# Optimization experiments

Measured on AMD Instinct MI355X. Metric: run time of the kernel, lower is better.

Reference implementation:

```python
import jax, jax.numpy as jnp
import numpy as np

NUM_HEAD = 16
D = 1024
HEAD_DIM = D // NUM_HEAD
EPS = 1e-5


def setup_inputs() -> dict:
    key = jax.random.key(0)
    ks = jax.random.split(key, 7)
    B, S = 2, 2048
    s = 1.0 / np.sqrt(D)
    return {
        "x": jax.random.normal(ks[0], (B, S, D), dtype=jnp.float32),
        "wq": jax.random.uniform(ks[1], (D, D), jnp.float32, -s, s),
        "bq": jax.random.uniform(ks[2], (D,), jnp.float32, -s, s),
        "wk": jax.random.uniform(ks[3], (D, D), jnp.float32, -s, s),
        "bk": jax.random.uniform(ks[4], (D,), jnp.float32, -s, s),
        "wv": jax.random.uniform(ks[5], (D, D), jnp.float32, -s, s),
        "bv": jax.random.uniform(ks[6], (D,), jnp.float32, -s, s),
        "gamma": jnp.ones((D,), jnp.float32),
        "beta": jnp.zeros((D,), jnp.float32),
    }


def reference(x, wq, bq, wk, bk, wv, bv, gamma, beta):
    B, S, Dm = x.shape
    # Linear: x @ W^T + b (torch convention), then split heads -> [B, H, S, hd]
    def proj(w, b):
        y = jnp.einsum("bsd,ed->bse", x, w) + b
        return y.reshape(B, S, NUM_HEAD, HEAD_DIM).transpose(0, 2, 1, 3)

    q = proj(wq, bq)
    k = proj(wk, bk)
    v = proj(wv, bv)

    scores = jnp.einsum("bhqd,bhkd->bhqk", q, k) / np.sqrt(HEAD_DIM).astype(x.dtype)
    attn = jax.nn.softmax(scores, axis=-1)
    out = jnp.einsum("bhqk,bhkd->bhqd", attn, v)
    out = out.transpose(0, 2, 1, 3).reshape(B, S, Dm)

    out = out + x
    mu = jnp.mean(out, axis=-1, keepdims=True)
    var = jnp.var(out, axis=-1, keepdims=True)
    out = (out - mu) * jax.lax.rsqrt(var + EPS) * gamma + beta
    return out
```

## Files before the change

### kernel.cpp

```cpp
#include <hip/hip_runtime.h>

typedef unsigned short u16;
typedef unsigned int   u32;
typedef __bf16 bf16x8 __attribute__((ext_vector_type(8)));
typedef float  f32x4  __attribute__((ext_vector_type(4)));

#define D_MODEL 1024
#define SEQ     2048
#define NHEAD   16
#define HD      64
#define SOFTMAX_SCL 0.18033688011112042f

__device__ __forceinline__ u16 f2bf(float f) {
    u32 u;
    __builtin_memcpy(&u, &f, 4);
    u32 r = (u + 0x7fffu + ((u >> 16) & 1u)) >> 16;
    return (u16)r;
}
__device__ __forceinline__ float bf2f(u16 v) {
    u32 u = ((u32)v) << 16;
    float f;
    __builtin_memcpy(&f, &u, 4);
    return f;
}

__device__ __forceinline__ void async_copy16(const u16* g, u16* l) {
    __builtin_amdgcn_global_load_lds(
        (__attribute__((address_space(1))) void*)g,
        (__attribute__((address_space(3))) void*)l, 16, 0, 0);
}

#define NX4 ((2 * SEQ * D_MODEL) / 4)
#define NW4 ((D_MODEL * D_MODEL) / 4)
__global__ __launch_bounds__(256) void conv_all(
    const float* __restrict__ x,  const float* __restrict__ wq,
    const float* __restrict__ wk, const float* __restrict__ wv,
    u16* __restrict__ xb, u16* __restrict__ wqb,
    u16* __restrict__ wkb, u16* __restrict__ wvb)
{
    int i = blockIdx.x * 256 + threadIdx.x;
    const float* src; u16* dst; int off;
    if (i < NX4)            { src = x;  dst = xb;  off = i; }
    else if (i < NX4 + NW4) { src = wq; dst = wqb; off = i - NX4; }
    else if (i < NX4 + 2 * NW4) { src = wk; dst = wkb; off = i - NX4 - NW4; }
    else                    { src = wv; dst = wvb; off = i - NX4 - 2 * NW4; }
    float4 a = ((const float4*)src)[off];
    ushort4 o;
    o.x = f2bf(a.x); o.y = f2bf(a.y); o.z = f2bf(a.z); o.w = f2bf(a.w);
    ((ushort4*)dst)[off] = o;
}

__global__ __launch_bounds__(256) void qkv_gemm(
    const u16* __restrict__ xb,
    const u16* __restrict__ wqb, const float* __restrict__ bq,
    const u16* __restrict__ wkb, const float* __restrict__ bk,
    const u16* __restrict__ wvb, const float* __restrict__ bv,
    u16* __restrict__ qb, u16* __restrict__ kb, u16* __restrict__ vt)
{
    const int bid  = blockIdx.x;
    const int pair = bid % 24;
    const int by   = bid / 24;
    const int z    = pair >> 3;
    const int bx   = pair & 7;

    const u16* Ap; const u16* Bp;
    int m0, n0;
    if (z < 2) {
        Ap = xb; Bp = (z == 1) ? wkb : wqb;
        m0 = by * 128;
        n0 = bx * 128;
    } else {
        Ap = wvb; Bp = xb;
        m0 = bx * 128;
        n0 = by * 128;
    }

    __shared__ u16 As[128 * 64];
    __shared__ u16 Bs[128 * 64];

    const int tid  = threadIdx.x;
    const int wave = tid >> 6;
    const int lane = tid & 63;
    const int quad = lane >> 4;
    const int l16  = lane & 15;
    const int wm   = wave >> 1;
    const int wn   = wave & 1;
    const int swz  = l16 & 7;

    int rr[4], co[4];
#pragma unroll
    for (int t = 0; t < 4; ++t) {
        int ch = (wave * 4 + t) * 64 + lane;
        rr[t] = ch >> 3;
        co[t] = ((ch & 7) ^ (rr[t] & 7)) * 8;
    }

    f32x4 acc[4][4] = {};

    for (int kt = 0; kt < D_MODEL; kt += 64) {
        __syncthreads();
#pragma unroll
        for (int t = 0; t < 4; ++t) {
            int chbase = (wave * 4 + t) * 64;
            async_copy16(Ap + (size_t)(m0 + rr[t]) * D_MODEL + kt + co[t], As + chbase * 8);
            async_copy16(Bp + (size_t)(n0 + rr[t]) * D_MODEL + kt + co[t], Bs + chbase * 8);
        }
        __syncthreads();

#pragma unroll
        for (int kc = 0; kc < 2; ++kc) {
            bf16x8 af[4], bf_[4];
#pragma unroll
            for (int i = 0; i < 4; ++i)
                af[i] = *(const bf16x8*)&As[(wm * 64 + i * 16 + l16) * 64 + (((kc * 4 + quad) ^ swz) << 3)];
#pragma unroll
            for (int j = 0; j < 4; ++j)
                bf_[j] = *(const bf16x8*)&Bs[(wn * 64 + j * 16 + l16) * 64 + (((kc * 4 + quad) ^ swz) << 3)];
#pragma unroll
            for (int i = 0; i < 4; ++i)
#pragma unroll
                for (int j = 0; j < 4; ++j)
                    acc[i][j] = __builtin_amdgcn_mfma_f32_16x16x32_bf16(af[i], bf_[j], acc[i][j], 0, 0, 0);
        }
    }

    if (z < 2) {
        u16* out = (z == 1) ? kb : qb;
        const float* bi = (z == 1) ? bk : bq;
        const float scl = (z == 1) ? 1.0f : SOFTMAX_SCL;
#pragma unroll
        for (int j = 0; j < 4; ++j) {
            int col = n0 + wn * 64 + j * 16 + l16;
            float bias = bi[col];
            int colbase = col & ~63;
            int dc  = (col >> 3) & 7;
            int dlo = col & 7;
#pragma unroll
            for (int i = 0; i < 4; ++i) {
#pragma unroll
                for (int r = 0; r < 4; ++r) {
                    int row = m0 + wm * 64 + i * 16 + quad * 4 + r;
                    size_t addr = (size_t)row * D_MODEL + colbase + ((dc ^ (row & 7)) << 3) + dlo;
                    out[addr] = f2bf((acc[i][j][r] + bias) * scl);
                }
            }
        }
    } else {
#pragma unroll
        for (int i = 0; i < 4; ++i) {
#pragma unroll
            for (int r = 0; r < 4; ++r) {
                int feat = m0 + wm * 64 + i * 16 + quad * 4 + r;
                float bias = bv[feat];
                int h = feat >> 6, d = feat & 63;
#pragma unroll
                for (int j = 0; j < 4; ++j) {
                    int tok = n0 + wn * 64 + j * 16 + l16;
                    int b = tok >> 11, s = tok & 2047;
                    size_t addr = ((size_t)(b * NHEAD + h) * HD + d) * SEQ
                                + (s & ~63) + (((((s >> 3) & 7) ^ (d & 7)) << 3)) + (s & 7);
                    vt[addr] = f2bf(acc[i][j][r] + bias);
                }
            }
        }
    }
}

__global__ __launch_bounds__(256) void attn_kernel(
    const u16* __restrict__ qb, const u16* __restrict__ kb, const u16* __restrict__ vtg,
    u16* __restrict__ abp, float* __restrict__ lsums)
{
    const int bid  = blockIdx.x;
    const int bh   = bid & 31;
    const int b    = bh >> 4;
    const int h    = bh & 15;
    const int q0   = ((bid >> 5) & 15) * 128;
    const int half = bid >> 9;

    const int tid  = threadIdx.x;
    const int wave = tid >> 6;
    const int lane = tid & 63;
    const int quad = lane >> 4;
    const int l16  = lane & 15;
    const int swz  = l16 & 7;

    __shared__ u16 Ks[4096];
    __shared__ u16 Vt[4096];
    __shared__ u16 Ps[8 * 1024];

    const size_t kbase = (size_t)b * SEQ * D_MODEL + h * 64;
    const size_t vbase = (size_t)(b * NHEAD + h) * HD * SEQ;

    bf16x8 aq[2][2];
#pragma unroll
    for (int rb = 0; rb < 2; ++rb) {
        const int qrow = q0 + wave * 32 + rb * 16 + l16;
        const u16* qrp = qb + (size_t)qrow * D_MODEL + h * 64;
        aq[rb][0] = *(const bf16x8*)(qrp + ((quad ^ swz) << 3));
        aq[rb][1] = *(const bf16x8*)(qrp + (((4 + quad) ^ swz) << 3));
    }

    const int r0 = tid >> 3, r1 = (tid + 256) >> 3;
    const int cs8 = (tid & 7) * 8;
    const u16* kg0 = kb + kbase + (size_t)(half * 1024 + r0) * D_MODEL + cs8;
    const u16* kg1 = kb + kbase + (size_t)(half * 1024 + r1) * D_MODEL + cs8;
    const u16* vg0 = vtg + vbase + (size_t)r0 * SEQ + half * 1024 + cs8;
    const u16* vg1 = vtg + vbase + (size_t)r1 * SEQ + half * 1024 + cs8;
    const int wofs = wave * 512;

    f32x4 oacc[2][4] = {};
    float lsum[2][4] = {};

    for (int t = 0; t < 16; ++t) {
        __syncthreads();
        async_copy16(kg0, Ks + wofs);
        async_copy16(kg1, Ks + 2048 + wofs);
        async_copy16(vg0, Vt + wofs);
        async_copy16(vg1, Vt + 2048 + wofs);
        kg0 += 64 * D_MODEL; kg1 += 64 * D_MODEL;
        vg0 += 64;           vg1 += 64;
        __syncthreads();

        f32x4 sacc[2][4] = {};
#pragma unroll
        for (int c = 0; c < 2; ++c) {
            bf16x8 bk_[4];
#pragma unroll
            for (int nb = 0; nb < 4; ++nb)
                bk_[nb] = *(const bf16x8*)&Ks[(nb * 16 + l16) * 64 + (((c * 4 + quad) ^ swz) << 3)];
#pragma unroll
            for (int rb = 0; rb < 2; ++rb)
#pragma unroll
                for (int nb = 0; nb < 4; ++nb)
                    sacc[rb][nb] = __builtin_amdgcn_mfma_f32_16x16x32_bf16(aq[rb][c], bk_[nb], sacc[rb][nb], 0, 0, 0);
        }

#pragma unroll
        for (int rb = 0; rb < 2; ++rb)
#pragma unroll
            for (int r = 0; r < 4; ++r)
#pragma unroll
                for (int nb = 0; nb < 4; ++nb) {
                    float e = exp2f(sacc[rb][nb][r]);
                    lsum[rb][r] += e;
                    u32 bits;
                    __builtin_memcpy(&bits, &e, 4);
                    Ps[wave * 2048 + rb * 1024 + r * 256 + nb * 64 + lane] = (u16)(bits >> 16);
                }

#pragma unroll
        for (int c = 0; c < 2; ++c) {
            bf16x8 ap[2];
#pragma unroll
            for (int rb = 0; rb < 2; ++rb)
                ap[rb] = *(const bf16x8*)&Ps[wave * 2048 + rb * 1024 + (l16 & 3) * 256
                                             + (c * 2 + (quad >> 1)) * 64
                                             + (l16 >> 2) * 16 + (quad & 1) * 8];
            bf16x8 bv_[4];
#pragma unroll
            for (int nb = 0; nb < 4; ++nb)
                bv_[nb] = *(const bf16x8*)&Vt[(nb * 16 + l16) * 64 + (((c * 4 + quad) ^ swz) << 3)];
#pragma unroll
            for (int rb = 0; rb < 2; ++rb)
#pragma unroll
                for (int nb = 0; nb < 4; ++nb)
                    oacc[rb][nb] = __builtin_amdgcn_mfma_f32_16x16x32_bf16(ap[rb], bv_[nb], oacc[rb][nb], 0, 0, 0);
        }
    }

#pragma unroll
    for (int rb = 0; rb < 2; ++rb)
#pragma unroll
        for (int r = 0; r < 4; ++r) {
            float s = lsum[rb][r];
            s += __shfl_xor(s, 1, 64);
            s += __shfl_xor(s, 2, 64);
            s += __shfl_xor(s, 4, 64);
            s += __shfl_xor(s, 8, 64);
            int row = q0 + wave * 32 + rb * 16 + quad * 4 + r;
            if (l16 == 0)
                lsums[((size_t)bh * 2 + half) * SEQ + row] = s;
#pragma unroll
            for (int nb = 0; nb < 4; ++nb) {
                int d = nb * 16 + l16;
                abp[(size_t)half * SEQ * 2 * D_MODEL
                    + ((size_t)b * SEQ + row) * D_MODEL + h * 64 + d] = f2bf(oacc[rb][nb][r]);
            }
        }
}

__global__ __launch_bounds__(256) void add_ln(
    const u16* __restrict__ abp, const float* __restrict__ lsums,
    const float* __restrict__ x,
    const float* __restrict__ gamma, const float* __restrict__ beta,
    float* __restrict__ out)
{
    const int row = blockIdx.x;
    const int tid = threadIdx.x;
    const size_t rb = (size_t)row * D_MODEL;
    const int b = row >> 11, s = row & 2047;
    const int h = tid >> 4;
    const int bh = b * NHEAD + h;

    float l = lsums[(size_t)bh * 2 * SEQ + s] + lsums[((size_t)bh * 2 + 1) * SEQ + s];
    float inv = 1.0f / l;

    uint2 a0 = ((const uint2*)(abp + rb))[tid];
    uint2 a1 = ((const uint2*)(abp + (size_t)SEQ * 2 * D_MODEL + rb))[tid];
    float4 xb = ((const float4*)(x + rb))[tid];

    float v[4];
    v[0] = (bf2f((u16)(a0.x & 0xffff)) + bf2f((u16)(a1.x & 0xffff))) * inv + xb.x;
    v[1] = (bf2f((u16)(a0.x >> 16))    + bf2f((u16)(a1.x >> 16)))    * inv + xb.y;
    v[2] = (bf2f((u16)(a0.y & 0xffff)) + bf2f((u16)(a1.y & 0xffff))) * inv + xb.z;
    v[3] = (bf2f((u16)(a0.y >> 16))    + bf2f((u16)(a1.y >> 16)))    * inv + xb.w;

    float sm  = v[0] + v[1] + v[2] + v[3];
    float s2 = v[0]*v[0] + v[1]*v[1] + v[2]*v[2] + v[3]*v[3];
#pragma unroll
    for (int off = 1; off < 64; off <<= 1) {
        sm += __shfl_xor(sm, off, 64);
        s2 += __shfl_xor(s2, off, 64);
    }

    __shared__ float red[2][4];
    int wave = tid >> 6, lane = tid & 63;
    if (lane == 0) { red[0][wave] = sm; red[1][wave] = s2; }
    __syncthreads();
    float st  = red[0][0] + red[0][1] + red[0][2] + red[0][3];
    float s2t = red[1][0] + red[1][1] + red[1][2] + red[1][3];

    float mu   = st * (1.0f / D_MODEL);
    float var  = s2t * (1.0f / D_MODEL) - mu * mu;
    float rstd = rsqrtf(var + 1e-5f);

    float4 g  = ((const float4*)(gamma))[tid];
    float4 bt = ((const float4*)(beta))[tid];
    float4 o;
    o.x = (v[0] - mu) * rstd * g.x + bt.x;
    o.y = (v[1] - mu) * rstd * g.y + bt.y;
    o.z = (v[2] - mu) * rstd * g.z + bt.z;
    o.w = (v[3] - mu) * rstd * g.w + bt.w;
    ((float4*)(out + rb))[tid] = o;
}

extern "C" void kernel_launch(void* const* d_in, const int* in_sizes, int n_in,
                              void* d_out, int out_size, void* d_ws, size_t ws_size,
                              hipStream_t stream) {
    const float* x     = (const float*)d_in[0];
    const float* wq    = (const float*)d_in[1];
    const float* bq    = (const float*)d_in[2];
    const float* wk    = (const float*)d_in[3];
    const float* bk    = (const float*)d_in[4];
    const float* wv    = (const float*)d_in[5];
    const float* bv    = (const float*)d_in[6];
    const float* gamma = (const float*)d_in[7];
    const float* beta  = (const float*)d_in[8];
    float* outp = (float*)d_out;

    char* ws = (char*)d_ws;
    u16*   xb    = (u16*)(ws);
    u16*   wqb   = (u16*)(ws + ((size_t)8  << 20));
    u16*   wkb   = (u16*)(ws + ((size_t)10 << 20));
    u16*   wvb   = (u16*)(ws + ((size_t)12 << 20));
    u16*   qb    = (u16*)(ws + ((size_t)16 << 20));
    u16*   kb    = (u16*)(ws + ((size_t)24 << 20));
    u16*   vt    = (u16*)(ws + ((size_t)32 << 20));
    u16*   abp   = (u16*)(ws + ((size_t)40 << 20));
    float* lsums = (float*)(ws + ((size_t)56 << 20));

    conv_all<<<dim3((NX4 + 3 * NW4) / 256), 256, 0, stream>>>(
        x, wq, wk, wv, xb, wqb, wkb, wvb);
    qkv_gemm<<<dim3(24 * 32), 256, 0, stream>>>(xb, wqb, bq, wkb, bk, wvb, bv, qb, kb, vt);
    attn_kernel<<<dim3(1024), 256, 0, stream>>>(qb, kb, vt, abp, lsums);
    add_ln<<<dim3(2 * SEQ), 256, 0, stream>>>(abp, lsums, x, gamma, beta, outp);
}
```

Before: 202.8 us.

## Compute transposed S=K·Q^T so P stores pack into swizzled vector LDS writes

Swaps the MFMA operands so each lane holds four consecutive key scores for one query row. Exp results can then be packed with byte-permute into 64-bit LDS stores into a swizzled P buffer. The rb loop is restructured so P is written and consumed per row block, which halves the P shared memory and allows the row sums to be reduced with two shuffles instead of four. The intent is to remove the scalar 16-bit LDS stores and shrink LDS usage, at the cost of a different MFMA ordering and risk of layout mistakes.

```diff
diff --git a/kernel.cpp b/kernel.cpp
--- a/kernel.cpp
+++ b/kernel.cpp
@@ -22,6 +22,11 @@
     float f;
     __builtin_memcpy(&f, &u, 4);
     return f;
+}
+__device__ __forceinline__ u32 fbits(float f) {
+    u32 u;
+    __builtin_memcpy(&u, &f, 4);
+    return u;
 }
 
 __device__ __forceinline__ void async_copy16(const u16* g, u16* l) {
@@ -183,10 +188,11 @@
     const int quad = lane >> 4;
     const int l16  = lane & 15;
     const int swz  = l16 & 7;
+    const int pswz = swz * 8;
 
     __shared__ u16 Ks[4096];
     __shared__ u16 Vt[4096];
-    __shared__ u16 Ps[8 * 1024];
+    __shared__ u16 Ps[4096];
 
     const size_t kbase = (size_t)b * SEQ * D_MODEL + h * 64;
     const size_t vbase = (size_t)(b * NHEAD + h) * HD * SEQ;
@@ -209,7 +215,7 @@
     const int wofs = wave * 512;
 
     f32x4 oacc[2][4] = {};
-    float lsum[2][4] = {};
+    float lsum[2] = {0.f, 0.f};
 
     for (int t = 0; t < 16; ++t) {
         __syncthreads();
@@ -221,65 +227,59 @@
         vg0 += 64;           vg1 += 64;
         __syncthreads();
 
-        f32x4 sacc[2][4] = {};
-#pragma unroll
-        for (int c = 0; c < 2; ++c) {
-            bf16x8 bk_[4];
-#pragma unroll
-            for (int nb = 0; nb < 4; ++nb)
-                bk_[nb] = *(const bf16x8*)&Ks[(nb * 16 + l16) * 64 + (((c * 4 + quad) ^ swz) << 3)];
-#pragma unroll
-            for (int rb = 0; rb < 2; ++rb)
-#pragma unroll
-                for (int nb = 0; nb < 4; ++nb)
-                    sacc[rb][nb] = __builtin_amdgcn_mfma_f32_16x16x32_bf16(aq[rb][c], bk_[nb], sacc[rb][nb], 0, 0, 0);
-        }
-
-#pragma unroll
-        for (int rb = 0; rb < 2; ++rb)
-#pragma unroll
-            for (int r = 0; r < 4; ++r)
+        bf16x8 kf[4][2];
+#pragma unroll
+        for (int kb2 = 0; kb2 < 4; ++kb2)
+#pragma unroll
+            for (int c = 0; c < 2; ++c)
+                kf[kb2][c] = *(const bf16x8*)&Ks[(kb2 * 16 + l16) * 64 + (((c * 4 + quad) ^ swz) << 3)];
+
+#pragma unroll
+        for (int rb = 0; rb < 2; ++rb) {
+            f32x4 sacc[4] = {};
+#pragma unroll
+            for (int kb2 = 0; kb2 < 4; ++kb2) {
+                sacc[kb2] = __builtin_amdgcn_mfma_f32_16x16x32_bf16(kf[kb2][0], aq[rb][0], sacc[kb2], 0, 0, 0);
+                sacc[kb2] = __builtin_amdgcn_mfma_f32_16x16x32_bf16(kf[kb2][1], aq[rb][1], sacc[kb2], 0, 0, 0);
+            }
+
+#pragma unroll
+            for (int kb2 = 0; kb2 < 4; ++kb2) {
+                float e0 = exp2f(sacc[kb2][0]);
+                float e1 = exp2f(sacc[kb2][1]);
+                float e2 = exp2f(sacc[kb2][2]);
+                float e3 = exp2f(sacc[kb2][3]);
+                lsum[rb] += (e0 + e1) + (e2 + e3);
+                u32 p0 = __builtin_amdgcn_perm(fbits(e1), fbits(e0), 0x07060302u);
+                u32 p1 = __builtin_amdgcn_perm(fbits(e3), fbits(e2), 0x07060302u);
+                int k0 = (kb2 * 16 + quad * 4) ^ pswz;
+                uint2 pk; pk.x = p0; pk.y = p1;
+                *(uint2*)&Ps[wave * 1024 + l16 * 64 + k0] = pk;
+            }
+
+#pragma unroll
+            for (int c = 0; c < 2; ++c) {
+                bf16x8 ap = *(const bf16x8*)&Ps[wave * 1024 + l16 * 64 + ((c * 32 + quad * 8) ^ pswz)];
 #pragma unroll
                 for (int nb = 0; nb < 4; ++nb) {
-                    float e = exp2f(sacc[rb][nb][r]);
-                    lsum[rb][r] += e;
-                    u32 bits;
-                    __builtin_memcpy(&bits, &e, 4);
-                    Ps[wave * 2048 + rb * 1024 + r * 256 + nb * 64 + lane] = (u16)(bits >> 16);
+                    bf16x8 vf = *(const bf16x8*)&Vt[(nb * 16 + l16) * 64 + (((c * 4 + quad) ^ swz) << 3)];
+                    oacc[rb][nb] = __builtin_amdgcn_mfma_f32_16x16x32_bf16(ap, vf, oacc[rb][nb], 0, 0, 0);
                 }
-
-#pragma unroll
-        for (int c = 0; c < 2; ++c) {
-            bf16x8 ap[2];
-#pragma unroll
-            for (int rb = 0; rb < 2; ++rb)
-                ap[rb] = *(const bf16x8*)&Ps[wave * 2048 + rb * 1024 + (l16 & 3) * 256
-                                             + (c * 2 + (quad >> 1)) * 64
-                                             + (l16 >> 2) * 16 + (quad & 1) * 8];
-            bf16x8 bv_[4];
-#pragma unroll
-            for (int nb = 0; nb < 4; ++nb)
-                bv_[nb] = *(const bf16x8*)&Vt[(nb * 16 + l16) * 64 + (((c * 4 + quad) ^ swz) << 3)];
-#pragma unroll
-            for (int rb = 0; rb < 2; ++rb)
-#pragma unroll
-                for (int nb = 0; nb < 4; ++nb)
-                    oacc[rb][nb] = __builtin_amdgcn_mfma_f32_16x16x32_bf16(ap[rb], bv_[nb], oacc[rb][nb], 0, 0, 0);
-        }
-    }
-
-#pragma unroll
-    for (int rb = 0; rb < 2; ++rb)
+            }
+        }
+    }
+
+#pragma unroll
+    for (int rb = 0; rb < 2; ++rb) {
+        float s = lsum[rb];
+        s += __shfl_xor(s, 16, 64);
+        s += __shfl_xor(s, 32, 64);
+        int qrow = q0 + wave * 32 + rb * 16 + l16;
+        if (quad == 0)
+            lsums[((size_t)bh * 2 + half) * SEQ + qrow] = s;
 #pragma unroll
         for (int r = 0; r < 4; ++r) {
-            float s = lsum[rb][r];
-            s += __shfl_xor(s, 1, 64);
-            s += __shfl_xor(s, 2, 64);
-            s += __shfl_xor(s, 4, 64);
-            s += __shfl_xor(s, 8, 64);
             int row = q0 + wave * 32 + rb * 16 + quad * 4 + r;
-            if (l16 == 0)
-                lsums[((size_t)bh * 2 + half) * SEQ + row] = s;
 #pragma unroll
             for (int nb = 0; nb < 4; ++nb) {
                 int d = nb * 16 + l16;
@@ -287,6 +287,7 @@
                     + ((size_t)b * SEQ + row) * D_MODEL + h * 64 + d] = f2bf(oacc[rb][nb][r]);
             }
         }
+    }
 }
 
 __global__ __launch_bounds__(256) void add_ln(
```

New measurement: 203.6 us. Within noise of the previous version (+0.4%).
